# Optimization experiments

Hardware: AMD Instinct MI355X
Metric: run time of the kernel (lower is better)

## Reference

```python
import jax, jax.numpy as jnp
import numpy as np

B, T, P = 16, 512, 2048
S_NUM, S_DEN = 256, 1024
DEN_SCALE = 1.0


def setup_inputs() -> dict:
    key = jax.random.key(0)
    ks = jax.random.split(key, 10)
    inp = {
        "input": jax.random.normal(ks[0], (B, T, P), dtype=jnp.float32),
        # lengths in [T//2, T] so every sequence is non-trivial
        "seqlengths": jax.random.randint(ks[1], (B,), T // 2, T + 1),
        "num_init": jax.random.normal(ks[2], (S_NUM,), dtype=jnp.float32),
        "num_trans": jax.nn.log_softmax(jax.random.normal(ks[3], (S_NUM, S_NUM), dtype=jnp.float32), axis=-1),
        "num_final": jax.random.normal(ks[4], (S_NUM,), dtype=jnp.float32),
        "num_pdf": jax.random.randint(ks[5], (S_NUM,), 0, P),
        "den_init": jax.random.normal(ks[6], (S_DEN,), dtype=jnp.float32),
        "den_trans": jax.nn.log_softmax(jax.random.normal(ks[7], (S_DEN, S_DEN), dtype=jnp.float32), axis=-1),
        "den_final": jax.random.normal(ks[8], (S_DEN,), dtype=jnp.float32),
        "den_pdf": jax.random.randint(ks[9], (S_DEN,), 0, P),
    }
    return inp


def _seq_logprob(loglikes, seqlengths, init, trans, final, pdf_ids):
    """Forward-algorithm log-marginal of each sequence under a dense FSM.

    loglikes: [B, T, P] frame pdf log-likelihoods
    Returns [B] log total probabilities.
    """
    emis = loglikes[:, :, pdf_ids]  # [B, T, S] state emissions via pdf gather
    alpha0 = init[None, :] + emis[:, 0, :]  # [B, S]

    def step(alpha, xt):
        t, e_t = xt  # e_t: [B, S]
        # alpha_new[b, s'] = logsumexp_s(alpha[b, s] + trans[s, s']) + e_t[b, s']
        a_new = jax.nn.logsumexp(alpha[:, :, None] + trans[None, :, :], axis=1) + e_t
        # freeze alpha once past each sequence's length
        alpha = jnp.where((t < seqlengths)[:, None], a_new, alpha)
        return alpha, None

    ts = jnp.arange(1, emis.shape[1])
    emis_t = jnp.moveaxis(emis[:, 1:, :], 1, 0)  # [T-1, B, S]
    alphaT, _ = jax.lax.scan(step, alpha0, (ts, emis_t))
    return jax.nn.logsumexp(alphaT + final[None, :], axis=-1)  # [B]


def reference(input, seqlengths, num_init, num_trans, num_final, num_pdf,
              den_init, den_trans, den_final, den_pdf):
    num_llh = jnp.sum(_seq_logprob(input, seqlengths, num_init, num_trans, num_final, num_pdf))
    den_llh = jnp.sum(_seq_logprob(input, seqlengths, den_init, den_trans, den_final, den_pdf))
    return -(num_llh - DEN_SCALE * den_llh)
```

## Files before the change

### kernel.cpp

```cpp
#include <hip/hip_runtime.h>

#define AG __HIP_MEMORY_SCOPE_AGENT
#define B_ 16
#define T_ 512
#define P_ 2048
#define SN_ 256
#define SD_ 1024
#define NGD 8
#define GB 16
#define NBD (NGD * GB)
#define NBLK (NBD + B_)
#define NTHR 1024
#define CHU 136

typedef unsigned long long u64;

__device__ __forceinline__ float alf(const float* p){ return __hip_atomic_load(p, __ATOMIC_RELAXED, AG); }
__device__ __forceinline__ void  asf(float* p, float v){ __hip_atomic_store(p, v, __ATOMIC_RELAXED, AG); }
__device__ __forceinline__ void  rsu(unsigned* p, unsigned v){ __hip_atomic_store(p, v, __ATOMIC_RELEASE, AG); }
__device__ __forceinline__ u64   ald64(const u64* p){ return __hip_atomic_load(p, __ATOMIC_RELAXED, AG); }
__device__ __forceinline__ void  ast64(u64* p, u64 v){ __hip_atomic_store(p, v, __ATOMIC_RELAXED, AG); }
__device__ __forceinline__ u64   pk(float v, unsigned t){ return ((u64)t << 32) | (u64)__float_as_uint(v); }
__device__ __forceinline__ void wait_eq(unsigned* p, unsigned v){
  while (__hip_atomic_load(p, __ATOMIC_RELAXED, AG) != v) __builtin_amdgcn_s_sleep(1);
  asm volatile("" ::: "memory");
}

__global__ void __attribute__((amdgpu_flat_work_group_size(1024, 1024)))
__attribute__((amdgpu_waves_per_eu(4, 4))) lfmmi_kernel(
    const float* __restrict__ input, const int* __restrict__ seqlen,
    const float* __restrict__ num_init, const float* __restrict__ num_trans,
    const float* __restrict__ num_final, const int* __restrict__ num_pdf,
    const float* __restrict__ den_init, const float* __restrict__ den_trans,
    const float* __restrict__ den_final, const int* __restrict__ den_pdf,
    float* __restrict__ out, float* __restrict__ ws)
{
  __shared__ __align__(16) unsigned char smem[25248];
  const int tid = threadIdx.x;
  const int bid = blockIdx.x;

  u64*      Qc     = (u64*)ws;
  float*    DenRes = (float*)(Qc + 2*NGD*GB*CHU);
  float*    NumRes = DenRes + 16;
  unsigned* DF     = (unsigned*)(NumRes + 16);
  unsigned* NF     = DF + NGD*16;

  const int wv = tid >> 6, ln = tid & 63;

  if (bid < NBD) {
    const int g = bid >> 4, r = bid & 15;
    const int col0 = r * 64;
    const int tm = ln >> 3, j8 = ln & 7;
    const int o  = 8 * wv + tm;
    const int ob = o >> 6, oc = o & 63;
    const bool lead = (j8 == 0);

    float* qsW = (float*)smem;
    float* red = (float*)(smem + 8704);
    float* Ms  = (float*)(smem + 25216);

    float wreg[64];
    {
      const float* wb = den_trans + (size_t)(64 * wv) * SD_ + col0 + ln;
      #pragma unroll
      for (int j = 0; j < 64; ++j) wreg[j] = __expf(wb[(size_t)j * SD_]);
    }

    const int b0 = 2 * g, b1 = 2 * g + 1;
    const size_t inb0 = (size_t)b0 * T_ * P_, inb1 = (size_t)b1 * T_ * P_;
    int pdfc = 0, slenL = 0; size_t inbL = 0;
    if (lead) {
      pdfc  = den_pdf[col0 + oc];
      inbL  = ob ? inb1 : inb0;
      slenL = seqlen[ob ? b1 : b0];
    }
    u64* myCh0 = Qc + ((size_t)(0 * NGD + g) * GB + r) * CHU;
    u64* myCh1 = Qc + ((size_t)(1 * NGD + g) * GB + r) * CHU;

    float v_prev = 0.f, Lr = 0.f;
    if (lead) {
      v_prev = __expf(den_init[col0 + oc] + input[inbL + pdfc]);
      ast64(myCh0 + o, pk(v_prev, 0u));
    }
    if (r == 0 && (wv == 0 || wv == 8)) {
      float mx = lead ? v_prev : 0.f;
      #pragma unroll
      for (int d = 1; d < 64; d <<= 1) mx = fmaxf(mx, __shfl_xor(mx, d));
      if (ln == 0) ast64(myCh0 + 128 + ob, pk(mx, 0u));
    }

    for (int t = 1; t <= 511; ++t) {
      const int pp = (t - 1) & 1, pc = t & 1;
      const unsigned et = (unsigned)(t - 1);
      float e = 0.f;
      if (lead) e = input[inbL + (size_t)t * P_ + pdfc];

      {
        const u64* chs = Qc + ((size_t)(pp * NGD + g) * GB + wv) * CHU;
        const u64* p0 = chs + ln;
        const u64* p1 = chs + 64 + ln;
        const bool pm = (wv == 0 && ln < 2);
        const u64* p2 = chs + 128 + ln;
        u64 x0 = ald64(p0);
        u64 x1 = ald64(p1);
        u64 x2 = pm ? ald64(p2) : 0;
        while ((unsigned)(x0 >> 32) != et) x0 = ald64(p0);
        qsW[wv * 136 + ln] = __uint_as_float((unsigned)x0);
        while ((unsigned)(x1 >> 32) != et) x1 = ald64(p1);
        qsW[wv * 136 + 64 + ln] = __uint_as_float((unsigned)x1);
        if (pm) {
          while ((unsigned)(x2 >> 32) != et) x2 = ald64(p2);
          Ms[pp * 2 + ln] = __uint_as_float((unsigned)x2);
        }
      }
      float a0 = 0.f, a1 = 0.f;
      {
        const float* qp = qsW + wv * 136;
        #pragma unroll
        for (int jj = 0; jj < 16; ++jj) {
          const float4 f0 = *(const float4*)(qp + 4 * jj);
          const float4 f1 = *(const float4*)(qp + 64 + 4 * jj);
          a0 = fmaf(f0.x, wreg[4*jj+0], a0); a0 = fmaf(f0.y, wreg[4*jj+1], a0);
          a0 = fmaf(f0.z, wreg[4*jj+2], a0); a0 = fmaf(f0.w, wreg[4*jj+3], a0);
          a1 = fmaf(f1.x, wreg[4*jj+0], a1); a1 = fmaf(f1.y, wreg[4*jj+1], a1);
          a1 = fmaf(f1.z, wreg[4*jj+2], a1); a1 = fmaf(f1.w, wreg[4*jj+3], a1);
        }
      }
      red[(pc * 16 + wv) * 129 + ln]      = a0;
      red[(pc * 16 + wv) * 129 + 64 + ln] = a1;
      __syncthreads();

      float acc = red[(pc * 16 + 2 * j8) * 129 + o]
                + red[(pc * 16 + 2 * j8 + 1) * 129 + o];
      acc += __shfl_xor(acc, 1);
      acc += __shfl_xor(acc, 2);
      acc += __shfl_xor(acc, 4);
      u64* myCh = pc ? myCh1 : myCh0;
      if (lead) {
        const float Mv = Ms[pp * 2 + ob];
        if (t < slenL) v_prev = (acc / Mv) * __expf(e);
        ast64(myCh + o, pk(v_prev, (unsigned)t));
      }
      if (r == 0 && (wv == 0 || wv == 8)) {
        float mx = lead ? v_prev : 0.f;
        #pragma unroll
        for (int d = 1; d < 64; d <<= 1) mx = fmaxf(mx, __shfl_xor(mx, d));
        if (ln == 0) {
          ast64(myCh + 128 + ob, pk(mx, (unsigned)t));
          if (t < slenL) Lr += __logf(Ms[pp * 2 + ob]);
        }
      }
    }

    if (r == 0) {
      __syncthreads();
      float* qf = (float*)smem;
      float* rs = (float*)(smem + 8192);
      {
        const u64* ch = Qc + ((size_t)(1 * NGD + g) * GB + wv) * CHU;
        const u64* p0 = ch + ln;
        const u64* p1 = ch + 64 + ln;
        u64 y0 = ald64(p0);
        u64 y1 = ald64(p1);
        while ((unsigned)(y0 >> 32) != 511u) y0 = ald64(p0);
        while ((unsigned)(y1 >> 32) != 511u) y1 = ald64(p1);
        qf[wv * 64 + ln]        = __uint_as_float((unsigned)y0);
        qf[1024 + wv * 64 + ln] = __uint_as_float((unsigned)y1);
      }
      __syncthreads();
      const int b2e = tid >> 9, ce = tid & 511;
      rs[tid] = qf[b2e * 1024 + ce] * __expf(den_final[ce])
              + qf[b2e * 1024 + 512 + ce] * __expf(den_final[512 + ce]);
      __syncthreads();
      for (int off = 256; off; off >>= 1) {
        const int base = (tid >= 512) ? 512 : 0, i = tid - base;
        if (i < off) rs[base + i] += rs[base + i + off];
        __syncthreads();
      }
      if (tid == 0)   asf(DenRes + 2 * g,     Lr + __logf(rs[0]));
      if (tid == 512) asf(DenRes + 2 * g + 1, Lr + __logf(rs[512]));
      __syncthreads();
      if (tid == 0) {
        rsu(DF + g * 16, 0x600D0000u | (unsigned)g);
        if (g == 0) {
          for (int g2 = 0; g2 < NGD; ++g2) wait_eq(DF + g2 * 16, 0x600D0000u | (unsigned)g2);
          for (int b2 = 0; b2 < B_; ++b2)  wait_eq(NF + b2 * 16, 0x600D0100u | (unsigned)b2);
          float sden = 0.f, snum = 0.f;
          for (int i = 0; i < 16; ++i) { sden += alf(DenRes + i); snum += alf(NumRes + i); }
          out[0] = -(snum - sden);
        }
      }
    }
  } else {
    const int b = bid - NBD;
    float* qn   = (float*)smem;
    float* redn = (float*)(smem + 2048);
    float* Ms2  = (float*)(smem + 18432);
    const size_t inb = (size_t)b * T_ * P_;
    const int slen = seqlen[b];

    float wn[64];
    {
      const float* wb = num_trans + (size_t)(wv * 16) * SN_ + ln;
      #pragma unroll
      for (int kk = 0; kk < 16; ++kk) {
        #pragma unroll
        for (int cc = 0; cc < 4; ++cc)
          wn[kk * 4 + cc] = __expf(wb[(size_t)kk * SN_ + 64 * cc]);
      }
    }
    int pdfn[4] = {0, 0, 0, 0};
    float Lr = 0.f;
    if (wv == 0) {
      #pragma unroll
      for (int cc = 0; cc < 4; ++cc) pdfn[cc] = num_pdf[ln + 64 * cc];
      float mx = 0.f;
      #pragma unroll
      for (int cc = 0; cc < 4; ++cc) {
        const float v = __expf(num_init[ln + 64 * cc] + input[inb + pdfn[cc]]);
        qn[ln + 64 * cc] = v;
        mx = fmaxf(mx, v);
      }
      #pragma unroll
      for (int d = 1; d < 64; d <<= 1) mx = fmaxf(mx, __shfl_xor(mx, d));
      if (ln == 0) Ms2[0] = mx;
    }
    __syncthreads();

    int tlast = 0;
    for (int t = 1; t <= 511; ++t) {
      if (t >= slen) break;
      tlast = t;
      const int pr = (t - 1) & 1, pw = t & 1;
      float e[4] = {0.f, 0.f, 0.f, 0.f};
      if (wv == 0) {
        #pragma unroll
        for (int cc = 0; cc < 4; ++cc) e[cc] = input[inb + (size_t)t * P_ + pdfn[cc]];
      }
      const float* qp = qn + pr * 256 + wv * 16;
      float ac[4] = {0.f, 0.f, 0.f, 0.f};
      #pragma unroll
      for (int jj = 0; jj < 4; ++jj) {
        const float4 f = *(const float4*)(qp + 4 * jj);
        #pragma unroll
        for (int cc = 0; cc < 4; ++cc) {
          ac[cc] = fmaf(f.x, wn[(4*jj+0)*4+cc], ac[cc]);
          ac[cc] = fmaf(f.y, wn[(4*jj+1)*4+cc], ac[cc]);
          ac[cc] = fmaf(f.z, wn[(4*jj+2)*4+cc], ac[cc]);
          ac[cc] = fmaf(f.w, wn[(4*jj+3)*4+cc], ac[cc]);
        }
      }
      #pragma unroll
      for (int cc = 0; cc < 4; ++cc) redn[wv * 256 + cc * 64 + ln] = ac[cc];
      __syncthreads();
      if (wv == 0) {
        float acc[4] = {0.f, 0.f, 0.f, 0.f};
        #pragma unroll
        for (int w = 0; w < 16; ++w) {
          #pragma unroll
          for (int cc = 0; cc < 4; ++cc) acc[cc] += redn[w * 256 + cc * 64 + ln];
        }
        const float Mv = Ms2[pr];
        const float rM = 1.0f / Mv;
        float mx = 0.f;
        #pragma unroll
        for (int cc = 0; cc < 4; ++cc) {
          const float v = acc[cc] * rM * __expf(e[cc]);
          qn[pw * 256 + ln + 64 * cc] = v;
          mx = fmaxf(mx, v);
        }
        #pragma unroll
        for (int d = 1; d < 64; d <<= 1) mx = fmaxf(mx, __shfl_xor(mx, d));
        if (ln == 0) { Ms2[pw] = mx; Lr += __logf(Mv); }
      }
      __syncthreads();
    }
    const int cur = tlast & 1;
    if (wv == 0) {
      float s = 0.f;
      #pragma unroll
      for (int cc = 0; cc < 4; ++cc)
        s += qn[cur * 256 + ln + 64 * cc] * __expf(num_final[ln + 64 * cc]);
      #pragma unroll
      for (int d = 1; d < 64; d <<= 1) s += __shfl_xor(s, d);
      if (ln == 0) {
        asf(NumRes + b, Lr + __logf(s));
        rsu(NF + b * 16, 0x600D0100u | (unsigned)b);
      }
    }
  }
}

extern "C" void kernel_launch(void* const* d_in, const int* in_sizes, int n_in,
                              void* d_out, int out_size, void* d_ws, size_t ws_size,
                              hipStream_t stream) {
  const float* input     = (const float*)d_in[0];
  const int*   seqlen    = (const int*)  d_in[1];
  const float* num_init  = (const float*)d_in[2];
  const float* num_trans = (const float*)d_in[3];
  const float* num_final = (const float*)d_in[4];
  const int*   num_pdf   = (const int*)  d_in[5];
  const float* den_init  = (const float*)d_in[6];
  const float* den_trans = (const float*)d_in[7];
  const float* den_final = (const float*)d_in[8];
  const int*   den_pdf   = (const int*)  d_in[9];
  float* out = (float*)d_out;
  float* ws  = (float*)d_ws;

  void* args[] = { &input, &seqlen, &num_init, &num_trans, &num_final, &num_pdf,
                   &den_init, &den_trans, &den_final, &den_pdf, &out, &ws };
  hipLaunchCooperativeKernel((void*)lfmmi_kernel, dim3(NBLK), dim3(NTHR),
                             args, 0, stream);
}
```

Baseline: 1.282 ms.

## Give each denominator group one sequence and double the group count

Each denominator group of 16 blocks now handles a single sequence instead of two, so there are 16 groups (256 blocks) plus the 16 numerator blocks. Per step every block does half the FMA work, exchanges half as much data through global memory, and uses a 16-lane reduction instead of an 8-lane one. The step tags are shifted by one so that a zeroed workspace is never mistaken for a valid value. The launch switches from hipLaunchCooperativeKernel to a plain launch, which drops the guarantee that all 272 spinning blocks are resident at once and could deadlock if they are not.

```diff
diff --git a/kernel.cpp b/kernel.cpp
--- a/kernel.cpp
+++ b/kernel.cpp
@@ -6,12 +6,12 @@
 #define P_ 2048
 #define SN_ 256
 #define SD_ 1024
-#define NGD 8
+#define NG 16
 #define GB 16
-#define NBD (NGD * GB)
+#define NBD (NG * GB)
 #define NBLK (NBD + B_)
 #define NTHR 1024
-#define CHU 136
+#define CHU 80
 
 typedef unsigned long long u64;
 
@@ -35,29 +35,28 @@
     const float* __restrict__ den_final, const int* __restrict__ den_pdf,
     float* __restrict__ out, float* __restrict__ ws)
 {
-  __shared__ __align__(16) unsigned char smem[25248];
+  __shared__ __align__(16) unsigned char smem[18464];
   const int tid = threadIdx.x;
   const int bid = blockIdx.x;
 
   u64*      Qc     = (u64*)ws;
-  float*    DenRes = (float*)(Qc + 2*NGD*GB*CHU);
+  float*    DenRes = (float*)(Qc + 2*NG*GB*CHU);
   float*    NumRes = DenRes + 16;
   unsigned* DF     = (unsigned*)(NumRes + 16);
-  unsigned* NF     = DF + NGD*16;
+  unsigned* NF     = DF + NG*16;
 
   const int wv = tid >> 6, ln = tid & 63;
 
   if (bid < NBD) {
     const int g = bid >> 4, r = bid & 15;
     const int col0 = r * 64;
-    const int tm = ln >> 3, j8 = ln & 7;
-    const int o  = 8 * wv + tm;
-    const int ob = o >> 6, oc = o & 63;
-    const bool lead = (j8 == 0);
+    const int tm = ln >> 4, j16 = ln & 15;
+    const int o  = 4 * wv + tm;
+    const bool lead = (j16 == 0);
 
     float* qsW = (float*)smem;
-    float* red = (float*)(smem + 8704);
-    float* Ms  = (float*)(smem + 25216);
+    float* red = (float*)(smem + 4096);
+    float* Ms  = (float*)(smem + 12672);
 
     float wreg[64];
     {
@@ -66,88 +65,79 @@
       for (int j = 0; j < 64; ++j) wreg[j] = __expf(wb[(size_t)j * SD_]);
     }
 
-    const int b0 = 2 * g, b1 = 2 * g + 1;
-    const size_t inb0 = (size_t)b0 * T_ * P_, inb1 = (size_t)b1 * T_ * P_;
-    int pdfc = 0, slenL = 0; size_t inbL = 0;
-    if (lead) {
-      pdfc  = den_pdf[col0 + oc];
-      inbL  = ob ? inb1 : inb0;
-      slenL = seqlen[ob ? b1 : b0];
-    }
-    u64* myCh0 = Qc + ((size_t)(0 * NGD + g) * GB + r) * CHU;
-    u64* myCh1 = Qc + ((size_t)(1 * NGD + g) * GB + r) * CHU;
+    const int slen = seqlen[g];
+    const size_t inb = (size_t)g * T_ * P_;
+    int pdfc = 0;
+    if (lead) pdfc = den_pdf[col0 + o];
+
+    u64* myCh0 = Qc + ((size_t)(0 * NG + g) * GB + r) * CHU;
+    u64* myCh1 = Qc + ((size_t)(1 * NG + g) * GB + r) * CHU;
 
     float v_prev = 0.f, Lr = 0.f;
     if (lead) {
-      v_prev = __expf(den_init[col0 + oc] + input[inbL + pdfc]);
-      ast64(myCh0 + o, pk(v_prev, 0u));
-    }
-    if (r == 0 && (wv == 0 || wv == 8)) {
+      v_prev = __expf(den_init[col0 + o] + input[inb + pdfc]);
+      ast64(myCh0 + o, pk(v_prev, 1u));
+    }
+    if (r == 0 && wv == 0) {
       float mx = lead ? v_prev : 0.f;
       #pragma unroll
       for (int d = 1; d < 64; d <<= 1) mx = fmaxf(mx, __shfl_xor(mx, d));
-      if (ln == 0) ast64(myCh0 + 128 + ob, pk(mx, 0u));
+      if (ln == 0) ast64(myCh0 + 64, pk(mx, 1u));
     }
 
     for (int t = 1; t <= 511; ++t) {
       const int pp = (t - 1) & 1, pc = t & 1;
-      const unsigned et = (unsigned)(t - 1);
+      const unsigned et = (unsigned)t;
       float e = 0.f;
-      if (lead) e = input[inbL + (size_t)t * P_ + pdfc];
+      if (lead) e = input[inb + (size_t)t * P_ + pdfc];
 
       {
-        const u64* chs = Qc + ((size_t)(pp * NGD + g) * GB + wv) * CHU;
+        const u64* chs = Qc + ((size_t)(pp * NG + g) * GB + wv) * CHU;
         const u64* p0 = chs + ln;
-        const u64* p1 = chs + 64 + ln;
-        const bool pm = (wv == 0 && ln < 2);
-        const u64* p2 = chs + 128 + ln;
+        const bool pm = (wv == 0 && ln == 0);
+        const u64* pM = chs + 64;
         u64 x0 = ald64(p0);
-        u64 x1 = ald64(p1);
-        u64 x2 = pm ? ald64(p2) : 0;
+        u64 xm = pm ? ald64(pM) : 0;
         while ((unsigned)(x0 >> 32) != et) x0 = ald64(p0);
-        qsW[wv * 136 + ln] = __uint_as_float((unsigned)x0);
-        while ((unsigned)(x1 >> 32) != et) x1 = ald64(p1);
-        qsW[wv * 136 + 64 + ln] = __uint_as_float((unsigned)x1);
+        qsW[wv * 64 + ln] = __uint_as_float((unsigned)x0);
         if (pm) {
-          while ((unsigned)(x2 >> 32) != et) x2 = ald64(p2);
-          Ms[pp * 2 + ln] = __uint_as_float((unsigned)x2);
-        }
-      }
-      float a0 = 0.f, a1 = 0.f;
+          while ((unsigned)(xm >> 32) != et) xm = ald64(pM);
+          Ms[pp] = __uint_as_float((unsigned)xm);
+        }
+      }
+      float a = 0.f;
       {
-        const float* qp = qsW + wv * 136;
+        const float* qp = qsW + wv * 64;
         #pragma unroll
         for (int jj = 0; jj < 16; ++jj) {
-          const float4 f0 = *(const float4*)(qp + 4 * jj);
-          const float4 f1 = *(const float4*)(qp + 64 + 4 * jj);
-          a0 = fmaf(f0.x, wreg[4*jj+0], a0); a0 = fmaf(f0.y, wreg[4*jj+1], a0);
-          a0 = fmaf(f0.z, wreg[4*jj+2], a0); a0 = fmaf(f0.w, wreg[4*jj+3], a0);
-          a1 = fmaf(f1.x, wreg[4*jj+0], a1); a1 = fmaf(f1.y, wreg[4*jj+1], a1);
-          a1 = fmaf(f1.z, wreg[4*jj+2], a1); a1 = fmaf(f1.w, wreg[4*jj+3], a1);
-        }
-      }
-      red[(pc * 16 + wv) * 129 + ln]      = a0;
-      red[(pc * 16 + wv) * 129 + 64 + ln] = a1;
-      __syncthreads();
-
-      float acc = red[(pc * 16 + 2 * j8) * 129 + o]
-                + red[(pc * 16 + 2 * j8 + 1) * 129 + o];
+          const float4 f = *(const float4*)(qp + 4 * jj);
+          a = fmaf(f.x, wreg[4*jj+0], a);
+          a = fmaf(f.y, wreg[4*jj+1], a);
+          a = fmaf(f.z, wreg[4*jj+2], a);
+          a = fmaf(f.w, wreg[4*jj+3], a);
+        }
+      }
+      red[(pc * 16 + wv) * 67 + ln] = a;
+      __syncthreads();
+
+      float acc = red[(pc * 16 + j16) * 67 + o];
       acc += __shfl_xor(acc, 1);
       acc += __shfl_xor(acc, 2);
       acc += __shfl_xor(acc, 4);
+      acc += __shfl_xor(acc, 8);
+      const float Mv = Ms[pp];
       u64* myCh = pc ? myCh1 : myCh0;
       if (lead) {
-        const float Mv = Ms[pp * 2 + ob];
-        if (t < slenL) v_prev = (acc / Mv) * __expf(e);
-        ast64(myCh + o, pk(v_prev, (unsigned)t));
-      }
-      if (r == 0 && (wv == 0 || wv == 8)) {
+        if (t < slen) v_prev = (acc / Mv) * __expf(e);
+        ast64(myCh + o, pk(v_prev, (unsigned)(t + 1)));
+      }
+      if (r == 0 && wv == 0) {
         float mx = lead ? v_prev : 0.f;
         #pragma unroll
         for (int d = 1; d < 64; d <<= 1) mx = fmaxf(mx, __shfl_xor(mx, d));
         if (ln == 0) {
-          ast64(myCh + 128 + ob, pk(mx, (unsigned)t));
-          if (t < slenL) Lr += __logf(Ms[pp * 2 + ob]);
+          ast64(myCh + 64, pk(mx, (unsigned)(t + 1)));
+          if (t < slen) Lr += __logf(Mv);
         }
       }
     }
@@ -155,35 +145,25 @@
     if (r == 0) {
       __syncthreads();
       float* qf = (float*)smem;
-      float* rs = (float*)(smem + 8192);
+      float* rs = (float*)(smem + 4096);
       {
-        const u64* ch = Qc + ((size_t)(1 * NGD + g) * GB + wv) * CHU;
-        const u64* p0 = ch + ln;
-        const u64* p1 = ch + 64 + ln;
-        u64 y0 = ald64(p0);
-        u64 y1 = ald64(p1);
-        while ((unsigned)(y0 >> 32) != 511u) y0 = ald64(p0);
-        while ((unsigned)(y1 >> 32) != 511u) y1 = ald64(p1);
-        qf[wv * 64 + ln]        = __uint_as_float((unsigned)y0);
-        qf[1024 + wv * 64 + ln] = __uint_as_float((unsigned)y1);
-      }
-      __syncthreads();
-      const int b2e = tid >> 9, ce = tid & 511;
-      rs[tid] = qf[b2e * 1024 + ce] * __expf(den_final[ce])
-              + qf[b2e * 1024 + 512 + ce] * __expf(den_final[512 + ce]);
-      __syncthreads();
-      for (int off = 256; off; off >>= 1) {
-        const int base = (tid >= 512) ? 512 : 0, i = tid - base;
-        if (i < off) rs[base + i] += rs[base + i + off];
+        const u64* pq = Qc + ((size_t)(1 * NG + g) * GB + wv) * CHU + ln;
+        u64 y = ald64(pq);
+        while ((unsigned)(y >> 32) != 512u) y = ald64(pq);
+        qf[wv * 64 + ln] = __uint_as_float((unsigned)y);
+      }
+      __syncthreads();
+      rs[tid] = qf[tid] * __expf(den_final[tid]);
+      __syncthreads();
+      for (int off = 512; off; off >>= 1) {
+        if (tid < off) rs[tid] += rs[tid + off];
         __syncthreads();
       }
-      if (tid == 0)   asf(DenRes + 2 * g,     Lr + __logf(rs[0]));
-      if (tid == 512) asf(DenRes + 2 * g + 1, Lr + __logf(rs[512]));
-      __syncthreads();
       if (tid == 0) {
+        asf(DenRes + g, Lr + __logf(rs[0]));
         rsu(DF + g * 16, 0x600D0000u | (unsigned)g);
         if (g == 0) {
-          for (int g2 = 0; g2 < NGD; ++g2) wait_eq(DF + g2 * 16, 0x600D0000u | (unsigned)g2);
+          for (int g2 = 0; g2 < NG; ++g2) wait_eq(DF + g2 * 16, 0x600D0000u | (unsigned)g2);
           for (int b2 = 0; b2 < B_; ++b2)  wait_eq(NF + b2 * 16, 0x600D0100u | (unsigned)b2);
           float sden = 0.f, snum = 0.f;
           for (int i = 0; i < 16; ++i) { sden += alf(DenRes + i); snum += alf(NumRes + i); }
@@ -307,8 +287,7 @@
   float* out = (float*)d_out;
   float* ws  = (float*)d_ws;
 
-  void* args[] = { &input, &seqlen, &num_init, &num_trans, &num_final, &num_pdf,
-                   &den_init, &den_trans, &den_final, &den_pdf, &out, &ws };
-  hipLaunchCooperativeKernel((void*)lfmmi_kernel, dim3(NBLK), dim3(NTHR),
-                             args, 0, stream);
+  lfmmi_kernel<<<dim3(NBLK), dim3(NTHR), 0, stream>>>(
+      input, seqlen, num_init, num_trans, num_final, num_pdf,
+      den_init, den_trans, den_final, den_pdf, out, ws);
 }
```

After: 1.582 ms. 23.4% more time.
